# Optimization experiments

Hardware: AMD Instinct MI355X
Metric: run time of the kernel (lower is better)

Reference implementation:

```python
import jax, jax.numpy as jnp
import numpy as np

T_SCALE = 10.0   # self.t = ones(1)*10
EPS = 1e-8       # torch cosine_similarity eps


def setup_inputs() -> dict:
    key = jax.random.key(0)
    k1, k2, k3 = jax.random.split(key, 3)
    B, D, C = 2048, 25088, 100
    feature = jax.random.normal(k1, (B, D), dtype=jnp.float32)
    label = jax.random.randint(k2, (B,), 0, C, dtype=jnp.int64)
    # mimic reset_parameters: uniform(-stdv, stdv), stdv = 1/sqrt(in_dim)
    stdv = 1.0 / np.sqrt(D)
    weight = jax.random.uniform(k3, (C, D), dtype=jnp.float32, minval=-stdv, maxval=stdv)
    return {"feature": feature, "label": label, "weight": weight}


def _cos_logits(feature, weight):
    # Equivalent to t * cosine_similarity over broadcasted (B, C, D):
    # L2-normalize rows (with torch's eps clamp on norms) then matmul.
    fn = feature / jnp.maximum(jnp.linalg.norm(feature, axis=-1, keepdims=True), EPS)
    wn = weight / jnp.maximum(jnp.linalg.norm(weight, axis=-1, keepdims=True), EPS)
    return T_SCALE * jnp.einsum('bd,cd->bc', fn, wn)  # [B, C]


def reference(feature, label, weight):
    pred = _cos_logits(feature, weight)                      # [B, C]
    logp = jax.nn.log_softmax(pred, axis=-1)
    valid = (label >= 0)
    safe_label = jnp.where(valid, label, 0)
    nll = -jnp.take_along_axis(logp, safe_label[:, None], axis=1)[:, 0]
    vmask = valid.astype(pred.dtype)
    n_valid = jnp.sum(vmask)
    loss = jnp.sum(nll * vmask) / jnp.maximum(n_valid, 1.0)  # CE with ignore_index=-1
    preds = jnp.argmax(pred, axis=1)
    acc = jnp.sum(vmask * (preds == label).astype(pred.dtype)) / (n_valid + 1e-10)
    return loss, acc
```

## Files before the change

### kernel.cpp

```cpp
#include <hip/hip_runtime.h>
#include <hip/hip_bf16.h>

#define D_DIM   25088
#define B_ROWS  2048
#define C_CLS   100
#define NT      7
#define NPAD    112
#define KSTEPS_TOTAL 784
#define EPS     1e-8f

typedef __bf16 bf16x8 __attribute__((ext_vector_type(8)));
typedef float  f32x4  __attribute__((ext_vector_type(4)));
typedef float  f32x2  __attribute__((ext_vector_type(2)));

__device__ __forceinline__ unsigned bfpack2(float lo, float hi) {
    unsigned a = __builtin_bit_cast(unsigned, lo);
    unsigned b = __builtin_bit_cast(unsigned, hi);
    a += 0x7FFFu + ((a >> 16) & 1u);
    b += 0x7FFFu + ((b >> 16) & 1u);
    return (a >> 16) | (b & 0xFFFF0000u);
}

__device__ __forceinline__ void gll16(const uint4* g, uint4* l) {
    __builtin_amdgcn_global_load_lds(
        (const __attribute__((address_space(1))) void*)g,
        (__attribute__((address_space(3))) void*)l, 16, 0, 0);
}

__global__ __launch_bounds__(256) void prep_kernel(const float* __restrict__ w,
                                                   float* __restrict__ wnorm2,
                                                   unsigned* __restrict__ wpack) {
    int c = blockIdx.x;
    int t = c >> 4, n = c & 15;
    bool real = (c < C_CLS);
    const float* row = w + (size_t)c * D_DIM;
    float s = 0.f;
    int i0 = blockIdx.y * 7;
#pragma unroll
    for (int ii = 0; ii < 7; ++ii) {
        int d = (i0 + ii) * 512 + threadIdx.x * 2;
        f32x2 v = {0.f, 0.f};
        if (real) v = *(const f32x2*)(row + d);
        s += v[0]*v[0] + v[1]*v[1];
        int gstep = d >> 5, r = d & 31, quad = r >> 3, j = r & 7;
        unsigned dw = bfpack2(v[0], v[1]);
        size_t idx = ((size_t)(gstep * 7 + t) * 64 + quad * 16 + n) * 4 + (j >> 1);
        wpack[idx] = dw;
    }
    if (!real) return;
    __shared__ float red[4];
    for (int o = 32; o; o >>= 1) s += __shfl_down(s, o, 64);
    if ((threadIdx.x & 63) == 0) red[threadIdx.x >> 6] = s;
    __syncthreads();
    if (threadIdx.x == 0) atomicAdd(&wnorm2[c], red[0] + red[1] + red[2] + red[3]);
}

__global__ __launch_bounds__(256, 4) void gemm_kernel(const float* __restrict__ feat,
                                                      const uint4* __restrict__ wpack,
                                                      float* __restrict__ pred2,
                                                      float* __restrict__ fnorm2s,
                                                      int ksteps) {
    __shared__ uint4 bst[2][NT * 64];

    int tid  = threadIdx.x;
    int wave = tid >> 6, lane = tid & 63;
    int m = lane & 15, quad = lane >> 4;
    int rowbase = blockIdx.x * 64 + wave * 16;
    int row = rowbase + m;
    int sidx = blockIdx.y;
    int gstep0 = sidx * ksteps;

    const float* pA = feat + (size_t)row * D_DIM + gstep0 * 32 + quad * 8;
    const uint4* qB = wpack + (size_t)gstep0 * NT * 64;

    f32x4 acc[NT];
#pragma unroll
    for (int t = 0; t < NT; ++t) acc[t] = (f32x4){0.f,0.f,0.f,0.f};
    float sumsq = 0.f;

    gll16(qB + wave * 64 + lane, &bst[0][wave * 64]);
    if (wave < 3) gll16(qB + (wave + 4) * 64 + lane, &bst[0][(wave + 4) * 64]);
    f32x4 a0 = ((const f32x4*)pA)[0], a1 = ((const f32x4*)pA)[1];
    __syncthreads();

    int cur = 0;
    for (int s = 0; s < ksteps; ++s) {
        const uint4* qn = qB + NT * 64;
        if (s + 1 < ksteps) {
            gll16(qn + wave * 64 + lane, &bst[cur ^ 1][wave * 64]);
            if (wave < 3) gll16(qn + (wave + 4) * 64 + lane, &bst[cur ^ 1][(wave + 4) * 64]);
        }
        const float* pn = pA + ((s + 1 < ksteps) ? 32 : 0);
        f32x4 n0 = ((const f32x4*)pn)[0];
        f32x4 n1 = ((const f32x4*)pn)[1];

        sumsq += a0[0]*a0[0] + a0[1]*a0[1] + a0[2]*a0[2] + a0[3]*a0[3]
               + a1[0]*a1[0] + a1[1]*a1[1] + a1[2]*a1[2] + a1[3]*a1[3];
        uint4 ap;
        ap.x = bfpack2(a0[0], a0[1]);
        ap.y = bfpack2(a0[2], a0[3]);
        ap.z = bfpack2(a1[0], a1[1]);
        ap.w = bfpack2(a1[2], a1[3]);
        bf16x8 afrag = __builtin_bit_cast(bf16x8, ap);
#pragma unroll
        for (int t = 0; t < NT; ++t) {
            uint4 bw = bst[cur][t * 64 + lane];
            acc[t] = __builtin_amdgcn_mfma_f32_16x16x32_bf16(
                afrag, __builtin_bit_cast(bf16x8, bw), acc[t], 0, 0, 0);
        }

        a0 = n0; a1 = n1;
        pA += 32; qB += NT * 64;
        __syncthreads();
        cur ^= 1;
    }

    sumsq += __shfl_xor(sumsq, 16, 64);
    sumsq += __shfl_xor(sumsq, 32, 64);
    if (lane < 16) fnorm2s[(size_t)sidx * B_ROWS + row] = sumsq;

    float* po = pred2 + ((size_t)sidx * B_ROWS + rowbase) * NPAD;
#pragma unroll
    for (int t = 0; t < NT; ++t) {
#pragma unroll
        for (int r = 0; r < 4; ++r) {
            po[(quad * 4 + r) * NPAD + t * 16 + m] = acc[t][r];
        }
    }
}

__global__ __launch_bounds__(256) void finalize_kernel(const float* __restrict__ pred2,
                                                       const float* __restrict__ fnorm2s,
                                                       const float* __restrict__ wnorm2,
                                                       const void* __restrict__ labp,
                                                       int lab64, int nsplit,
                                                       float4* __restrict__ rowred) {
    int gwave = (blockIdx.x * 256 + threadIdx.x) >> 6;
    int lane = threadIdx.x & 63;
    int row = gwave;
    if (row >= B_ROWS) return;

    float fn2 = (lane < nsplit) ? fnorm2s[(size_t)lane * B_ROWS + row] : 0.f;
    for (int o = 1; o < 64; o <<= 1) fn2 += __shfl_xor(fn2, o, 64);
    float finv = 10.0f / fmaxf(sqrtf(fn2), EPS);

    float s0 = 0.f, s1 = 0.f;
    for (int s = 0; s < nsplit; ++s) {
        const float* pr = pred2 + ((size_t)s * B_ROWS + row) * NPAD;
        s0 += pr[lane];
        if (lane < NPAD - 64) s1 += pr[64 + lane];
    }
    int c0 = lane, c1 = lane + 64;
    float l0 = s0 * (1.0f / fmaxf(sqrtf(wnorm2[c0]), EPS)) * finv;
    float l1 = -1e30f;
    if (c1 < C_CLS) l1 = s1 * (1.0f / fmaxf(sqrtf(wnorm2[c1]), EPS)) * finv;

    float mx = l0; int am = c0;
    if (l1 > mx) { mx = l1; am = c1; }
    for (int o = 1; o < 64; o <<= 1) {
        float om = __shfl_xor(mx, o, 64);
        int   oa = __shfl_xor(am, o, 64);
        if (om > mx || (om == mx && oa < am)) { mx = om; am = oa; }
    }
    float se = expf(l0 - mx) + expf(l1 - mx);
    for (int o = 1; o < 64; o <<= 1) se += __shfl_xor(se, o, 64);

    int lab = lab64 ? (int)((const long long*)labp)[row] : ((const int*)labp)[row];
    int labc = (lab < 0) ? 0 : lab;
    float lv = (labc >= 64) ? l1 : l0;
    float ll = __shfl(lv, labc & 63, 64);

    if (lane == 0) {
        float lse = mx + logf(se);
        bool valid = (lab >= 0);
        float4 o;
        o.x = valid ? (lse - ll) : 0.f;
        o.y = (valid && am == lab) ? 1.f : 0.f;
        o.z = valid ? 1.f : 0.f;
        o.w = 0.f;
        rowred[row] = o;
    }
}

__global__ __launch_bounds__(256) void reduce_kernel(const float4* __restrict__ rowred,
                                                     float* __restrict__ out) {
    float nll = 0.f, cor = 0.f, val = 0.f;
    for (int i = threadIdx.x; i < B_ROWS; i += 256) {
        float4 v = rowred[i];
        nll += v.x; cor += v.y; val += v.z;
    }
    for (int o = 32; o; o >>= 1) {
        nll += __shfl_down(nll, o, 64);
        cor += __shfl_down(cor, o, 64);
        val += __shfl_down(val, o, 64);
    }
    __shared__ float r[3][4];
    int w = threadIdx.x >> 6;
    if ((threadIdx.x & 63) == 0) { r[0][w] = nll; r[1][w] = cor; r[2][w] = val; }
    __syncthreads();
    if (threadIdx.x == 0) {
        float N = r[0][0] + r[0][1] + r[0][2] + r[0][3];
        float C = r[1][0] + r[1][1] + r[1][2] + r[1][3];
        float V = r[2][0] + r[2][1] + r[2][2] + r[2][3];
        out[0] = N / fmaxf(V, 1.0f);
        out[1] = C / (V + 1e-10f);
    }
}

extern "C" void kernel_launch(void* const* d_in, const int* in_sizes, int n_in,
                              void* d_out, int out_size, void* d_ws, size_t ws_size,
                              hipStream_t stream) {
    const float* feat   = (const float*)d_in[0];
    const void*  label  = d_in[1];
    const float* weight = (const float*)d_in[2];
    float* out = (float*)d_out;

    char* ws = (char*)d_ws;
    float*  wnorm2  = (float*)(ws);
    float4* rowred  = (float4*)(ws + 512);
    uint4*  wpack   = (uint4*)(ws + 33792);
    float*  fnorm2s = (float*)(ws + 5653504);
    float*  pred2   = (float*)(ws + 5882880);

    int nsplit = 28;
    {
        const int cand[5] = {28, 8, 4, 2, 1};
        for (int i = 0; i < 5; ++i) {
            nsplit = cand[i];
            size_t need = 5882880 + (size_t)nsplit * B_ROWS * NPAD * 4;
            if (need <= ws_size) break;
        }
    }
    int ksteps = KSTEPS_TOTAL / nsplit;

    int lab64 = (n_in > 1 && in_sizes[1] >= B_ROWS * 8) ? 1 : 0;

    hipMemsetAsync(ws, 0, 448, stream);
    prep_kernel<<<dim3(NPAD, 7), 256, 0, stream>>>(weight, wnorm2, (unsigned*)wpack);
    gemm_kernel<<<dim3(B_ROWS / 64, nsplit), 256, 0, stream>>>(feat, wpack, pred2, fnorm2s, ksteps);
    finalize_kernel<<<B_ROWS / 4, 256, 0, stream>>>(pred2, fnorm2s, wnorm2, label, lab64, nsplit, rowred);
    reduce_kernel<<<1, 256, 0, stream>>>(rowred, out);
}
```

Measured before the change: 325.7 us.

## Double rows per wave to reuse B tile, raise split-K, drop atomics

Each wave now computes two 16-row M tiles against the same LDS-staged weight fragment, which halves the weight LDS traffic per MFMA and halves the blocks along M. The split-K factor rises to 56 with a compile-time step count so the loop can fully unroll and occupancy stays up. The weight-norm atomics and the memset are replaced by per-slice partial sums that finalize adds up. In exchange, partial-product memory doubles and finalize reads more data, and register pressure roughly doubles for the accumulators.

```diff
diff --git a/kernel.cpp b/kernel.cpp
--- a/kernel.cpp
+++ b/kernel.cpp
@@ -28,7 +28,7 @@
 }
 
 __global__ __launch_bounds__(256) void prep_kernel(const float* __restrict__ w,
-                                                   float* __restrict__ wnorm2,
+                                                   float* __restrict__ wnorm2p,
                                                    unsigned* __restrict__ wpack) {
     int c = blockIdx.x;
     int t = c >> 4, n = c & 15;
@@ -47,91 +47,112 @@
         size_t idx = ((size_t)(gstep * 7 + t) * 64 + quad * 16 + n) * 4 + (j >> 1);
         wpack[idx] = dw;
     }
-    if (!real) return;
     __shared__ float red[4];
     for (int o = 32; o; o >>= 1) s += __shfl_down(s, o, 64);
     if ((threadIdx.x & 63) == 0) red[threadIdx.x >> 6] = s;
     __syncthreads();
-    if (threadIdx.x == 0) atomicAdd(&wnorm2[c], red[0] + red[1] + red[2] + red[3]);
-}
-
+    if (threadIdx.x == 0) wnorm2p[blockIdx.y * NPAD + c] = red[0] + red[1] + red[2] + red[3];
+}
+
+template<int KS>
 __global__ __launch_bounds__(256, 4) void gemm_kernel(const float* __restrict__ feat,
                                                       const uint4* __restrict__ wpack,
                                                       float* __restrict__ pred2,
-                                                      float* __restrict__ fnorm2s,
-                                                      int ksteps) {
+                                                      float* __restrict__ fnorm2s) {
     __shared__ uint4 bst[2][NT * 64];
 
     int tid  = threadIdx.x;
     int wave = tid >> 6, lane = tid & 63;
     int m = lane & 15, quad = lane >> 4;
-    int rowbase = blockIdx.x * 64 + wave * 16;
-    int row = rowbase + m;
+    int rowbase = blockIdx.x * 128 + wave * 32;
+    int row0 = rowbase + m;
+    int row1 = rowbase + 16 + m;
     int sidx = blockIdx.y;
-    int gstep0 = sidx * ksteps;
-
-    const float* pA = feat + (size_t)row * D_DIM + gstep0 * 32 + quad * 8;
+    int gstep0 = sidx * KS;
+
+    const float* pA0 = feat + (size_t)row0 * D_DIM + gstep0 * 32 + quad * 8;
+    const float* pA1 = feat + (size_t)row1 * D_DIM + gstep0 * 32 + quad * 8;
     const uint4* qB = wpack + (size_t)gstep0 * NT * 64;
 
-    f32x4 acc[NT];
-#pragma unroll
-    for (int t = 0; t < NT; ++t) acc[t] = (f32x4){0.f,0.f,0.f,0.f};
-    float sumsq = 0.f;
+    f32x4 acc0[NT], acc1[NT];
+#pragma unroll
+    for (int t = 0; t < NT; ++t) {
+        acc0[t] = (f32x4){0.f,0.f,0.f,0.f};
+        acc1[t] = (f32x4){0.f,0.f,0.f,0.f};
+    }
+    float ss0 = 0.f, ss1 = 0.f;
 
     gll16(qB + wave * 64 + lane, &bst[0][wave * 64]);
     if (wave < 3) gll16(qB + (wave + 4) * 64 + lane, &bst[0][(wave + 4) * 64]);
-    f32x4 a0 = ((const f32x4*)pA)[0], a1 = ((const f32x4*)pA)[1];
+    f32x4 a00 = ((const f32x4*)pA0)[0], a01 = ((const f32x4*)pA0)[1];
+    f32x4 a10 = ((const f32x4*)pA1)[0], a11 = ((const f32x4*)pA1)[1];
     __syncthreads();
 
     int cur = 0;
-    for (int s = 0; s < ksteps; ++s) {
+#pragma unroll
+    for (int s = 0; s < KS; ++s) {
         const uint4* qn = qB + NT * 64;
-        if (s + 1 < ksteps) {
+        if (s + 1 < KS) {
             gll16(qn + wave * 64 + lane, &bst[cur ^ 1][wave * 64]);
             if (wave < 3) gll16(qn + (wave + 4) * 64 + lane, &bst[cur ^ 1][(wave + 4) * 64]);
         }
-        const float* pn = pA + ((s + 1 < ksteps) ? 32 : 0);
-        f32x4 n0 = ((const f32x4*)pn)[0];
-        f32x4 n1 = ((const f32x4*)pn)[1];
-
-        sumsq += a0[0]*a0[0] + a0[1]*a0[1] + a0[2]*a0[2] + a0[3]*a0[3]
-               + a1[0]*a1[0] + a1[1]*a1[1] + a1[2]*a1[2] + a1[3]*a1[3];
-        uint4 ap;
-        ap.x = bfpack2(a0[0], a0[1]);
-        ap.y = bfpack2(a0[2], a0[3]);
-        ap.z = bfpack2(a1[0], a1[1]);
-        ap.w = bfpack2(a1[2], a1[3]);
-        bf16x8 afrag = __builtin_bit_cast(bf16x8, ap);
+        int adv = (s + 1 < KS) ? 32 : 0;
+        f32x4 n00 = ((const f32x4*)(pA0 + adv))[0];
+        f32x4 n01 = ((const f32x4*)(pA0 + adv))[1];
+        f32x4 n10 = ((const f32x4*)(pA1 + adv))[0];
+        f32x4 n11 = ((const f32x4*)(pA1 + adv))[1];
+
+        ss0 += a00[0]*a00[0] + a00[1]*a00[1] + a00[2]*a00[2] + a00[3]*a00[3]
+             + a01[0]*a01[0] + a01[1]*a01[1] + a01[2]*a01[2] + a01[3]*a01[3];
+        ss1 += a10[0]*a10[0] + a10[1]*a10[1] + a10[2]*a10[2] + a10[3]*a10[3]
+             + a11[0]*a11[0] + a11[1]*a11[1] + a11[2]*a11[2] + a11[3]*a11[3];
+        uint4 ap0, ap1;
+        ap0.x = bfpack2(a00[0], a00[1]);
+        ap0.y = bfpack2(a00[2], a00[3]);
+        ap0.z = bfpack2(a01[0], a01[1]);
+        ap0.w = bfpack2(a01[2], a01[3]);
+        ap1.x = bfpack2(a10[0], a10[1]);
+        ap1.y = bfpack2(a10[2], a10[3]);
+        ap1.z = bfpack2(a11[0], a11[1]);
+        ap1.w = bfpack2(a11[2], a11[3]);
+        bf16x8 af0 = __builtin_bit_cast(bf16x8, ap0);
+        bf16x8 af1 = __builtin_bit_cast(bf16x8, ap1);
 #pragma unroll
         for (int t = 0; t < NT; ++t) {
-            uint4 bw = bst[cur][t * 64 + lane];
-            acc[t] = __builtin_amdgcn_mfma_f32_16x16x32_bf16(
-                afrag, __builtin_bit_cast(bf16x8, bw), acc[t], 0, 0, 0);
-        }
-
-        a0 = n0; a1 = n1;
-        pA += 32; qB += NT * 64;
+            bf16x8 bf = __builtin_bit_cast(bf16x8, bst[cur][t * 64 + lane]);
+            acc0[t] = __builtin_amdgcn_mfma_f32_16x16x32_bf16(af0, bf, acc0[t], 0, 0, 0);
+            acc1[t] = __builtin_amdgcn_mfma_f32_16x16x32_bf16(af1, bf, acc1[t], 0, 0, 0);
+        }
+
+        a00 = n00; a01 = n01; a10 = n10; a11 = n11;
+        pA0 += 32; pA1 += 32; qB += NT * 64;
         __syncthreads();
         cur ^= 1;
     }
 
-    sumsq += __shfl_xor(sumsq, 16, 64);
-    sumsq += __shfl_xor(sumsq, 32, 64);
-    if (lane < 16) fnorm2s[(size_t)sidx * B_ROWS + row] = sumsq;
+    ss0 += __shfl_xor(ss0, 16, 64);
+    ss0 += __shfl_xor(ss0, 32, 64);
+    ss1 += __shfl_xor(ss1, 16, 64);
+    ss1 += __shfl_xor(ss1, 32, 64);
+    if (lane < 16) {
+        fnorm2s[(size_t)sidx * B_ROWS + row0] = ss0;
+        fnorm2s[(size_t)sidx * B_ROWS + row1] = ss1;
+    }
 
     float* po = pred2 + ((size_t)sidx * B_ROWS + rowbase) * NPAD;
 #pragma unroll
     for (int t = 0; t < NT; ++t) {
 #pragma unroll
         for (int r = 0; r < 4; ++r) {
-            po[(quad * 4 + r) * NPAD + t * 16 + m] = acc[t][r];
+            po[(quad * 4 + r) * NPAD + t * 16 + m]        = acc0[t][r];
+            po[(16 + quad * 4 + r) * NPAD + t * 16 + m]   = acc1[t][r];
         }
     }
 }
 
 __global__ __launch_bounds__(256) void finalize_kernel(const float* __restrict__ pred2,
                                                        const float* __restrict__ fnorm2s,
-                                                       const float* __restrict__ wnorm2,
+                                                       const float* __restrict__ wnorm2p,
                                                        const void* __restrict__ labp,
                                                        int lab64, int nsplit,
                                                        float4* __restrict__ rowred) {
@@ -151,9 +172,15 @@
         if (lane < NPAD - 64) s1 += pr[64 + lane];
     }
     int c0 = lane, c1 = lane + 64;
-    float l0 = s0 * (1.0f / fmaxf(sqrtf(wnorm2[c0]), EPS)) * finv;
+    float wn0 = 0.f, wn1 = 0.f;
+#pragma unroll
+    for (int j = 0; j < 7; ++j) {
+        wn0 += wnorm2p[j * NPAD + c0];
+        if (c1 < C_CLS) wn1 += wnorm2p[j * NPAD + c1];
+    }
+    float l0 = s0 * (1.0f / fmaxf(sqrtf(wn0), EPS)) * finv;
     float l1 = -1e30f;
-    if (c1 < C_CLS) l1 = s1 * (1.0f / fmaxf(sqrtf(wnorm2[c1]), EPS)) * finv;
+    if (c1 < C_CLS) l1 = s1 * (1.0f / fmaxf(sqrtf(wn1), EPS)) * finv;
 
     float mx = l0; int am = c0;
     if (l1 > mx) { mx = l1; am = c1; }
@@ -216,28 +243,34 @@
     float* out = (float*)d_out;
 
     char* ws = (char*)d_ws;
-    float*  wnorm2  = (float*)(ws);
-    float4* rowred  = (float4*)(ws + 512);
-    uint4*  wpack   = (uint4*)(ws + 33792);
-    float*  fnorm2s = (float*)(ws + 5653504);
-    float*  pred2   = (float*)(ws + 5882880);
-
-    int nsplit = 28;
+    float*  wnorm2p = (float*)(ws);
+    float4* rowred  = (float4*)(ws + 3328);
+    uint4*  wpack   = (uint4*)(ws + 36352);
+    float*  fnorm2s = (float*)(ws + 5656064);
+    float*  pred2   = (float*)(ws + 6114816);
+
+    int nsplit = 56;
     {
-        const int cand[5] = {28, 8, 4, 2, 1};
-        for (int i = 0; i < 5; ++i) {
+        const int cand[6] = {56, 28, 14, 4, 2, 1};
+        for (int i = 0; i < 6; ++i) {
             nsplit = cand[i];
-            size_t need = 5882880 + (size_t)nsplit * B_ROWS * NPAD * 4;
+            size_t need = 6114816 + (size_t)nsplit * B_ROWS * NPAD * 4;
             if (need <= ws_size) break;
         }
     }
-    int ksteps = KSTEPS_TOTAL / nsplit;
 
     int lab64 = (n_in > 1 && in_sizes[1] >= B_ROWS * 8) ? 1 : 0;
 
-    hipMemsetAsync(ws, 0, 448, stream);
-    prep_kernel<<<dim3(NPAD, 7), 256, 0, stream>>>(weight, wnorm2, (unsigned*)wpack);
-    gemm_kernel<<<dim3(B_ROWS / 64, nsplit), 256, 0, stream>>>(feat, wpack, pred2, fnorm2s, ksteps);
-    finalize_kernel<<<B_ROWS / 4, 256, 0, stream>>>(pred2, fnorm2s, wnorm2, label, lab64, nsplit, rowred);
+    prep_kernel<<<dim3(NPAD, 7), 256, 0, stream>>>(weight, wnorm2p, (unsigned*)wpack);
+    dim3 ggrid(B_ROWS / 128, nsplit);
+    switch (nsplit) {
+        case 56: gemm_kernel<14> <<<ggrid, 256, 0, stream>>>(feat, wpack, pred2, fnorm2s); break;
+        case 28: gemm_kernel<28> <<<ggrid, 256, 0, stream>>>(feat, wpack, pred2, fnorm2s); break;
+        case 14: gemm_kernel<56> <<<ggrid, 256, 0, stream>>>(feat, wpack, pred2, fnorm2s); break;
+        case 4:  gemm_kernel<196><<<ggrid, 256, 0, stream>>>(feat, wpack, pred2, fnorm2s); break;
+        case 2:  gemm_kernel<392><<<ggrid, 256, 0, stream>>>(feat, wpack, pred2, fnorm2s); break;
+        default: gemm_kernel<784><<<ggrid, 256, 0, stream>>>(feat, wpack, pred2, fnorm2s); break;
+    }
+    finalize_kernel<<<B_ROWS / 4, 256, 0, stream>>>(pred2, fnorm2s, wnorm2p, label, lab64, nsplit, rowred);
     reduce_kernel<<<1, 256, 0, stream>>>(rowred, out);
 }
```

After: 436.9 us. 1.34x slower.
